# Performance work log

Hardware: AMD Instinct MI355X
Metric: run time of the kernel (lower is better)

The kernel has to match this reference:

```python
import jax, jax.numpy as jnp
import numpy as np

SLOT_DIM = 128
HIDDEN = 64


def setup_inputs() -> dict:
    key = jax.random.key(0)
    k1, k2, k3, k4, k5 = jax.random.split(key, 5)
    b, k, d, h = 64, 128, SLOT_DIM, HIDDEN
    slots = jax.random.normal(k1, (b, k, d), dtype=jnp.float32)
    # edge_mlp params: Linear(2d -> h), Linear(h -> 1)
    s1 = 1.0 / np.sqrt(2 * d)
    W1 = jax.random.uniform(k2, (h, 2 * d), minval=-s1, maxval=s1, dtype=jnp.float32)
    b1 = jax.random.uniform(k3, (h,), minval=-s1, maxval=s1, dtype=jnp.float32)
    s2 = 1.0 / np.sqrt(h)
    W2 = jax.random.uniform(k4, (h,), minval=-s2, maxval=s2, dtype=jnp.float32)
    b2 = jax.random.uniform(k5, (), minval=-s2, maxval=s2, dtype=jnp.float32)
    return {"slots": slots, "W1": W1, "b1": b1, "W2": W2, "b2": b2}


def reference(slots, W1, b1, W2, b2):
    # slots: (b,k,d). Original concatenates [left,right] along features then
    # applies Linear(2d->h). Equivalent (same math): split W1 into halves and
    # broadcast-add, avoiding the (b,k,k,2d) concat tensor.
    b, k, d = slots.shape
    left_h = jnp.einsum('bkd,hd->bkh', slots, W1[:, :d])   # (b,k,h)
    right_h = jnp.einsum('bkd,hd->bkh', slots, W1[:, d:])  # (b,k,h)
    hidden = jax.nn.relu(left_h[:, :, None, :] + right_h[:, None, :, :] + b1)  # (b,k,k,h)
    logits = jnp.einsum('bijh,h->bij', hidden, W2) + b2    # (b,k,k)
    adj = jax.nn.sigmoid(logits)
    eye = jnp.eye(k, dtype=adj.dtype)[None]
    return adj * (1.0 - eye)
```

## Files before the change

### kernel.cpp

```cpp
#include <hip/hip_runtime.h>

#define BB 64
#define KK 128
#define DD 128

typedef __attribute__((ext_vector_type(8))) short bf16x8;
typedef __attribute__((ext_vector_type(4))) float f32x4;
typedef _Float16 half2v __attribute__((ext_vector_type(2)));
typedef __fp16 fp16x2 __attribute__((ext_vector_type(2)));

__device__ __forceinline__ unsigned cvt_pk_bf16(float x, float y) {
    unsigned r;
    asm("v_cvt_pk_bf16_f32 %0, %1, %2" : "=v"(r) : "v"(x), "v"(y));
    return r;
}

__device__ __forceinline__ unsigned cvt_pkrtz_u(float x, float y) {
    const fp16x2 pk = __builtin_amdgcn_cvt_pkrtz(x, y);
    return __builtin_bit_cast(unsigned, pk);
}

__device__ __forceinline__ unsigned pk_add_relu(unsigned a, unsigned b) {
    unsigned s, r;
    asm("v_pk_add_f16 %0, %1, %2" : "=v"(s) : "v"(a), "v"(b));
    asm("v_pk_max_f16 %0, %1, 0" : "=v"(r) : "v"(s));
    return r;
}

__device__ __forceinline__ float dot2acc(unsigned a, unsigned b, float c) {
#if __has_builtin(__builtin_amdgcn_fdot2)
    return __builtin_amdgcn_fdot2(__builtin_bit_cast(half2v, a),
                                  __builtin_bit_cast(half2v, b), c, false);
#else
    float r;
    asm("v_dot2_f32_f16 %0, %1, %2, %3" : "=v"(r) : "v"(a), "v"(b), "v"(c));
    return r;
#endif
}

__global__ __launch_bounds__(512, 2) void fused_kernel(
    const float* __restrict__ slots, const float* __restrict__ W1,
    const float* __restrict__ b1, const float* __restrict__ W2,
    const float* __restrict__ b2p, float* __restrict__ out)
{
    __shared__ unsigned smem_w[16384];
    char* smem = (char*)smem_w;

    const int t   = threadIdx.x;
    const int blk = blockIdx.x;
    const int b   = blk >> 2;
    const int it  = (blk >> 1) & 1;
    const int jt  = blk & 1;

    const int lane = t & 63;
    const int w    = t >> 6;
    const int lr   = lane & 15;
    const int lk   = lane >> 4;
    const int side = w >> 2;
    const int hq   = w & 3;

    const float badd = (side == 0) ? b1[hq * 16 + lr] : 0.0f;
    float w2lo = 0.f, w2hi = 0.f;
    if (t < 32) {
        const int hl = (t & 15) + 32 * (t >> 4);
        w2lo = W2[hl]; w2hi = W2[hl + 16];
    }

    {
        const float* srcI = slots + ((size_t)(b * KK) + it * 64) * DD;
        const float* srcJ = slots + ((size_t)(b * KK) + jt * 64) * DD;
#pragma unroll
        for (int x0 = 0; x0 < 2048; x0 += 512) {
            const int x = x0 + t;
            const int row = x >> 4, cb = x & 15;
            const float* src = (row < 64 ? srcI + row * DD
                                         : srcJ + (row - 64) * DD) + cb * 8;
            const float4 f0 = *reinterpret_cast<const float4*>(src);
            const float4 f1 = *reinterpret_cast<const float4*>(src + 4);
            uint4 pk;
            pk.x = cvt_pk_bf16(f0.x, f0.y); pk.y = cvt_pk_bf16(f0.z, f0.w);
            pk.z = cvt_pk_bf16(f1.x, f1.y); pk.w = cvt_pk_bf16(f1.z, f1.w);
            *reinterpret_cast<uint4*>(smem + row * 256 + ((cb ^ (row & 7)) << 4)) = pk;
        }
#pragma unroll
        for (int x0 = 0; x0 < 2048; x0 += 512) {
            const int x = x0 + t;
            const int row = x >> 5, cb = x & 31;
            const float* src = W1 + row * 256 + cb * 8;
            const float4 f0 = *reinterpret_cast<const float4*>(src);
            const float4 f1 = *reinterpret_cast<const float4*>(src + 4);
            uint4 pk;
            pk.x = cvt_pk_bf16(f0.x, f0.y); pk.y = cvt_pk_bf16(f0.z, f0.w);
            pk.z = cvt_pk_bf16(f1.x, f1.y); pk.w = cvt_pk_bf16(f1.z, f1.w);
            *reinterpret_cast<uint4*>(smem + 32768 + row * 512 + ((cb ^ (row & 7)) << 4)) = pk;
        }
    }
    __syncthreads();

    bf16x8 bfr[4];
#pragma unroll
    for (int kf = 0; kf < 4; ++kf) {
        const int rowB = hq * 16 + lr;
        const int cb   = side * 16 + kf * 4 + lk;
        bfr[kf] = *reinterpret_cast<const bf16x8*>(
            smem + 32768 + rowB * 512 + ((cb ^ (rowB & 7)) << 4));
    }
    f32x4 acc[4];
#pragma unroll
    for (int m = 0; m < 4; ++m) acc[m] = f32x4{0.f, 0.f, 0.f, 0.f};
#pragma unroll
    for (int m = 0; m < 4; ++m) {
#pragma unroll
        for (int kf = 0; kf < 4; ++kf) {
            const int row = side * 64 + 16 * m + lr;
            const int cb  = kf * 4 + lk;
            const bf16x8 af = *reinterpret_cast<const bf16x8*>(
                smem + row * 256 + ((cb ^ (row & 7)) << 4));
            acc[m] = __builtin_amdgcn_mfma_f32_16x16x32_bf16(af, bfr[kf], acc[m], 0, 0, 0);
        }
    }
    __syncthreads();

    {
        __fp16* dst = (__fp16*)smem + (side ? 4608 : 0);
        const int g  = hq >> 1;
        const int hl = hq & 1;
#pragma unroll
        for (int m = 0; m < 4; ++m)
#pragma unroll
            for (int r = 0; r < 4; ++r) {
                const int row = 16 * m + 4 * lk + r;
                dst[(row * 36 + g * 16 + lr) * 2 + hl] = (__fp16)(acc[m][r] + badd);
            }
        if (t < 32) ((unsigned*)smem)[4608 + t] = cvt_pkrtz_u(w2lo, w2hi);
    }
    __syncthreads();

    const int tx = t & 15;
    const int ty = t >> 4;
    const unsigned* LsP = (const unsigned*)smem;
    const unsigned* RsP = LsP + 2304;
    const unsigned* W2p = LsP + 4608;

    uint4 w2r[8];
#pragma unroll
    for (int s = 0; s < 8; ++s)
        w2r[s] = *reinterpret_cast<const uint4*>(W2p + s * 4);

    float pacc[2][4] = {};
    uint4 l4a[2], r4a[4], l4b[2], r4b[4];

#define LD_STEP(L4, R4, s)                                                        \
    {                                                                             \
        _Pragma("unroll") for (int ii = 0; ii < 2; ++ii)                          \
            L4[ii] = *reinterpret_cast<const uint4*>(LsP + (ty + 32 * ii) * 36 + (s) * 4); \
        _Pragma("unroll") for (int jj = 0; jj < 4; ++jj)                          \
            R4[jj] = *reinterpret_cast<const uint4*>(RsP + (tx + 16 * jj) * 36 + (s) * 4); \
    }

#define COMPUTE_STEP(L4, R4, s)                                                   \
    {                                                                             \
        _Pragma("unroll") for (int ii = 0; ii < 2; ++ii)                          \
        _Pragma("unroll") for (int jj = 0; jj < 4; ++jj) {                        \
            float a = pacc[ii][jj];                                               \
            a = dot2acc(pk_add_relu(L4[ii].x, R4[jj].x), w2r[s].x, a);            \
            a = dot2acc(pk_add_relu(L4[ii].y, R4[jj].y), w2r[s].y, a);            \
            a = dot2acc(pk_add_relu(L4[ii].z, R4[jj].z), w2r[s].z, a);            \
            a = dot2acc(pk_add_relu(L4[ii].w, R4[jj].w), w2r[s].w, a);            \
            pacc[ii][jj] = a;                                                     \
        }                                                                         \
    }

    LD_STEP(l4a, r4a, 0)
#pragma unroll
    for (int sp = 0; sp < 4; ++sp) {
        LD_STEP(l4b, r4b, 2 * sp + 1)
        COMPUTE_STEP(l4a, r4a, 2 * sp)
        if (sp < 3) LD_STEP(l4a, r4a, 2 * sp + 2)
        COMPUTE_STEP(l4b, r4b, 2 * sp + 1)
    }
#undef LD_STEP
#undef COMPUTE_STEP

    const float b2 = *b2p;
#pragma unroll
    for (int ii = 0; ii < 2; ++ii) {
        const int gi = it * 64 + ty + 32 * ii;
        float* orow = out + ((size_t)(b * KK) + gi) * KK + jt * 64;
#pragma unroll
        for (int jj = 0; jj < 4; ++jj) {
            const int jl = tx + 16 * jj;
            const int gj = jt * 64 + jl;
            const float xv = pacc[ii][jj] + b2;
            const float sg = 1.0f / (1.0f + __expf(-xv));
            orow[jl] = (gi == gj) ? 0.0f : sg;
        }
    }
}

extern "C" void kernel_launch(void* const* d_in, const int* in_sizes, int n_in,
                              void* d_out, int out_size, void* d_ws, size_t ws_size,
                              hipStream_t stream) {
    const float* slots = (const float*)d_in[0];
    const float* W1    = (const float*)d_in[1];
    const float* b1    = (const float*)d_in[2];
    const float* W2    = (const float*)d_in[3];
    const float* b2    = (const float*)d_in[4];
    float* out = (float*)d_out;
    (void)d_ws; (void)ws_size; (void)in_sizes; (void)n_in; (void)out_size;

    fused_kernel<<<BB * 4, 512, 0, stream>>>(slots, W1, b1, W2, b2, out);
}
```

Measured before the change: 12.56 us.

## Split into 512 smaller blocks with W1 fragments loaded straight to registers

The grid doubles to 512 blocks of 256 threads, each owning a 64x32 output tile instead of 64x64. W1 B-fragments are now loaded from global memory directly into registers, which removes the W1 shared-memory staging and one barrier and shrinks LDS use. Each wave computes two h-column fragments so the MFMA phase covers all 64 hidden units with 4 waves, and the right side only projects its 32 rows. The cost is more redundant projection of the I-side rows and more repeated W1 global reads across blocks.

```diff
diff --git a/kernel.cpp b/kernel.cpp
--- a/kernel.cpp
+++ b/kernel.cpp
@@ -38,39 +38,56 @@
 #endif
 }
 
-__global__ __launch_bounds__(512, 2) void fused_kernel(
+__global__ __launch_bounds__(256, 2) void fused_kernel(
     const float* __restrict__ slots, const float* __restrict__ W1,
     const float* __restrict__ b1, const float* __restrict__ W2,
     const float* __restrict__ b2p, float* __restrict__ out)
 {
-    __shared__ unsigned smem_w[16384];
+    __shared__ unsigned smem_w[9632];
     char* smem = (char*)smem_w;
 
     const int t   = threadIdx.x;
     const int blk = blockIdx.x;
-    const int b   = blk >> 2;
-    const int it  = (blk >> 1) & 1;
-    const int jt  = blk & 1;
+    const int b   = blk >> 3;
+    const int it  = (blk >> 2) & 1;
+    const int jt  = blk & 3;
 
     const int lane = t & 63;
     const int w    = t >> 6;
     const int lr   = lane & 15;
     const int lk   = lane >> 4;
-    const int side = w >> 2;
-    const int hq   = w & 3;
-
-    const float badd = (side == 0) ? b1[hq * 16 + lr] : 0.0f;
+    const int side = w >> 1;
+    const int grp  = w & 1;
+
+    const float b2 = *b2p;
+    const float b1lo = (side == 0) ? b1[grp * 32 + lr]      : 0.0f;
+    const float b1hi = (side == 0) ? b1[grp * 32 + 16 + lr] : 0.0f;
     float w2lo = 0.f, w2hi = 0.f;
     if (t < 32) {
         const int hl = (t & 15) + 32 * (t >> 4);
         w2lo = W2[hl]; w2hi = W2[hl + 16];
     }
 
+    bf16x8 bfr[2][4];
+#pragma unroll
+    for (int n = 0; n < 2; ++n)
+#pragma unroll
+        for (int kf = 0; kf < 4; ++kf) {
+            const int rowB = grp * 32 + n * 16 + lr;
+            const float* p = W1 + rowB * 256 + side * 128 + kf * 32 + lk * 8;
+            const float4 f0 = *reinterpret_cast<const float4*>(p);
+            const float4 f1 = *reinterpret_cast<const float4*>(p + 4);
+            uint4 pk;
+            pk.x = cvt_pk_bf16(f0.x, f0.y); pk.y = cvt_pk_bf16(f0.z, f0.w);
+            pk.z = cvt_pk_bf16(f1.x, f1.y); pk.w = cvt_pk_bf16(f1.z, f1.w);
+            bfr[n][kf] = __builtin_bit_cast(bf16x8, pk);
+        }
+
     {
         const float* srcI = slots + ((size_t)(b * KK) + it * 64) * DD;
-        const float* srcJ = slots + ((size_t)(b * KK) + jt * 64) * DD;
-#pragma unroll
-        for (int x0 = 0; x0 < 2048; x0 += 512) {
+        const float* srcJ = slots + ((size_t)(b * KK) + jt * 32) * DD;
+#pragma unroll
+        for (int x0 = 0; x0 < 1536; x0 += 256) {
             const int x = x0 + t;
             const int row = x >> 4, cb = x & 15;
             const float* src = (row < 64 ? srcI + row * DD
@@ -82,86 +99,73 @@
             pk.z = cvt_pk_bf16(f1.x, f1.y); pk.w = cvt_pk_bf16(f1.z, f1.w);
             *reinterpret_cast<uint4*>(smem + row * 256 + ((cb ^ (row & 7)) << 4)) = pk;
         }
-#pragma unroll
-        for (int x0 = 0; x0 < 2048; x0 += 512) {
-            const int x = x0 + t;
-            const int row = x >> 5, cb = x & 31;
-            const float* src = W1 + row * 256 + cb * 8;
-            const float4 f0 = *reinterpret_cast<const float4*>(src);
-            const float4 f1 = *reinterpret_cast<const float4*>(src + 4);
-            uint4 pk;
-            pk.x = cvt_pk_bf16(f0.x, f0.y); pk.y = cvt_pk_bf16(f0.z, f0.w);
-            pk.z = cvt_pk_bf16(f1.x, f1.y); pk.w = cvt_pk_bf16(f1.z, f1.w);
-            *reinterpret_cast<uint4*>(smem + 32768 + row * 512 + ((cb ^ (row & 7)) << 4)) = pk;
-        }
     }
     __syncthreads();
 
-    bf16x8 bfr[4];
-#pragma unroll
-    for (int kf = 0; kf < 4; ++kf) {
-        const int rowB = hq * 16 + lr;
-        const int cb   = side * 16 + kf * 4 + lk;
-        bfr[kf] = *reinterpret_cast<const bf16x8*>(
-            smem + 32768 + rowB * 512 + ((cb ^ (rowB & 7)) << 4));
-    }
-    f32x4 acc[4];
-#pragma unroll
-    for (int m = 0; m < 4; ++m) acc[m] = f32x4{0.f, 0.f, 0.f, 0.f};
+    f32x4 acc[4][2];
+#pragma unroll
+    for (int m = 0; m < 4; ++m)
+#pragma unroll
+        for (int n = 0; n < 2; ++n) acc[m][n] = f32x4{0.f, 0.f, 0.f, 0.f};
+
 #pragma unroll
     for (int m = 0; m < 4; ++m) {
+        if (side == 1 && m >= 2) continue;
 #pragma unroll
         for (int kf = 0; kf < 4; ++kf) {
             const int row = side * 64 + 16 * m + lr;
             const int cb  = kf * 4 + lk;
             const bf16x8 af = *reinterpret_cast<const bf16x8*>(
                 smem + row * 256 + ((cb ^ (row & 7)) << 4));
-            acc[m] = __builtin_amdgcn_mfma_f32_16x16x32_bf16(af, bfr[kf], acc[m], 0, 0, 0);
-        }
-    }
-    __syncthreads();
+#pragma unroll
+            for (int n = 0; n < 2; ++n)
+                acc[m][n] = __builtin_amdgcn_mfma_f32_16x16x32_bf16(
+                    af, bfr[n][kf], acc[m][n], 0, 0, 0);
+        }
+    }
 
     {
-        __fp16* dst = (__fp16*)smem + (side ? 4608 : 0);
-        const int g  = hq >> 1;
-        const int hl = hq & 1;
-#pragma unroll
-        for (int m = 0; m < 4; ++m)
+        unsigned* dst = smem_w + (side ? 8448 : 6144);
+#pragma unroll
+        for (int m = 0; m < 4; ++m) {
+            if (side == 1 && m >= 2) continue;
 #pragma unroll
             for (int r = 0; r < 4; ++r) {
                 const int row = 16 * m + 4 * lk + r;
-                dst[(row * 36 + g * 16 + lr) * 2 + hl] = (__fp16)(acc[m][r] + badd);
+                dst[row * 36 + grp * 16 + lr] =
+                    cvt_pkrtz_u(acc[m][0][r] + b1lo, acc[m][1][r] + b1hi);
             }
-        if (t < 32) ((unsigned*)smem)[4608 + t] = cvt_pkrtz_u(w2lo, w2hi);
+        }
+        if (t < 32) smem_w[9600 + t] = cvt_pkrtz_u(w2lo, w2hi);
     }
     __syncthreads();
 
     const int tx = t & 15;
     const int ty = t >> 4;
-    const unsigned* LsP = (const unsigned*)smem;
-    const unsigned* RsP = LsP + 2304;
-    const unsigned* W2p = LsP + 4608;
+    const unsigned* LsP = smem_w + 6144;
+    const unsigned* RsP = smem_w + 8448;
+    const unsigned* W2p = smem_w + 9600;
 
     uint4 w2r[8];
 #pragma unroll
     for (int s = 0; s < 8; ++s)
         w2r[s] = *reinterpret_cast<const uint4*>(W2p + s * 4);
 
-    float pacc[2][4] = {};
-    uint4 l4a[2], r4a[4], l4b[2], r4b[4];
+    float pacc[4][2] = {};
+    uint4 l4a[4], r4a[2], l4b[4], r4b[2];
 
 #define LD_STEP(L4, R4, s)                                                        \
     {                                                                             \
-        _Pragma("unroll") for (int ii = 0; ii < 2; ++ii)                          \
-            L4[ii] = *reinterpret_cast<const uint4*>(LsP + (ty + 32 * ii) * 36 + (s) * 4); \
-        _Pragma("unroll") for (int jj = 0; jj < 4; ++jj)                          \
+        _Pragma("unroll") for (int ii = 0; ii < 4; ++ii)                          \
+            L4[ii] = *reinterpret_cast<const uint4*>(LsP + (ty + 16 * ii) * 36 + (s) * 4); \
+        _Pragma("unroll") for (int jj = 0; jj < 2; ++jj)                          \
             R4[jj] = *reinterpret_cast<const uint4*>(RsP + (tx + 16 * jj) * 36 + (s) * 4); \
     }
 
 #define COMPUTE_STEP(L4, R4, s)                                                   \
     {                                                                             \
-        _Pragma("unroll") for (int ii = 0; ii < 2; ++ii)                          \
-        _Pragma("unroll") for (int jj = 0; jj < 4; ++jj) {                        \
+        _Pragma("unroll") for (int ii = 0; ii < 4; ++ii)                          \
+        _Pragma("unroll") for (int jj = 0; jj < 2; ++jj) {                        \
             float a = pacc[ii][jj];                                               \
             a = dot2acc(pk_add_relu(L4[ii].x, R4[jj].x), w2r[s].x, a);            \
             a = dot2acc(pk_add_relu(L4[ii].y, R4[jj].y), w2r[s].y, a);            \
@@ -182,15 +186,14 @@
 #undef LD_STEP
 #undef COMPUTE_STEP
 
-    const float b2 = *b2p;
-#pragma unroll
-    for (int ii = 0; ii < 2; ++ii) {
-        const int gi = it * 64 + ty + 32 * ii;
-        float* orow = out + ((size_t)(b * KK) + gi) * KK + jt * 64;
-#pragma unroll
-        for (int jj = 0; jj < 4; ++jj) {
+#pragma unroll
+    for (int ii = 0; ii < 4; ++ii) {
+        const int gi = it * 64 + ty + 16 * ii;
+        float* orow = out + ((size_t)(b * KK) + gi) * KK + jt * 32;
+#pragma unroll
+        for (int jj = 0; jj < 2; ++jj) {
             const int jl = tx + 16 * jj;
-            const int gj = jt * 64 + jl;
+            const int gj = jt * 32 + jl;
             const float xv = pacc[ii][jj] + b2;
             const float sg = 1.0f / (1.0f + __expf(-xv));
             orow[jl] = (gi == gj) ? 0.0f : sg;
@@ -209,5 +212,5 @@
     float* out = (float*)d_out;
     (void)d_ws; (void)ws_size; (void)in_sizes; (void)n_in; (void)out_size;
 
-    fused_kernel<<<BB * 4, 512, 0, stream>>>(slots, W1, b1, W2, b2, out);
-}
+    fused_kernel<<<BB * 8, 256, 0, stream>>>(slots, W1, b1, W2, b2, out);
+}
```

After: 14.88 us. +18.4%, slower.

## Load W1 fragments directly into registers and retile MFMA to drop a barrier

Applied to the files above, without the earlier changes.

Each wave now loads its W1 B-fragments straight from global memory into registers, so W1 is no longer staged through shared memory. The MFMA work is retiled so each wave computes a 32x32 output block (2x2 fragments) instead of a 64x16 one. The half-precision L/R results go to a separate shared region, which removes the barrier between the MFMA reads and the writes, and a packed conversion replaces the scalar fp16 stores. This shrinks LDS use and removes one synchronization, at the cost of redundant uncoalesced global W1 reads across blocks and more registers held.

```diff
diff --git a/kernel.cpp b/kernel.cpp
--- a/kernel.cpp
+++ b/kernel.cpp
@@ -43,7 +43,7 @@
     const float* __restrict__ b1, const float* __restrict__ W2,
     const float* __restrict__ b2p, float* __restrict__ out)
 {
-    __shared__ unsigned smem_w[16384];
+    __shared__ unsigned smem_w[12832];
     char* smem = (char*)smem_w;
 
     const int t   = threadIdx.x;
@@ -57,14 +57,32 @@
     const int lr   = lane & 15;
     const int lk   = lane >> 4;
     const int side = w >> 2;
-    const int hq   = w & 3;
-
-    const float badd = (side == 0) ? b1[hq * 16 + lr] : 0.0f;
-    float w2lo = 0.f, w2hi = 0.f;
+    const int grp  = (w >> 1) & 1;
+    const int mh   = w & 1;
+
+    const float b2v  = *b2p;
+    const float b1lo = (side == 0) ? b1[grp * 32 + lr]      : 0.0f;
+    const float b1hi = (side == 0) ? b1[grp * 32 + 16 + lr] : 0.0f;
+
     if (t < 32) {
         const int hl = (t & 15) + 32 * (t >> 4);
-        w2lo = W2[hl]; w2hi = W2[hl + 16];
-    }
+        smem_w[12800 + t] = cvt_pkrtz_u(W2[hl], W2[hl + 16]);
+    }
+
+    bf16x8 bfr[2][4];
+#pragma unroll
+    for (int n = 0; n < 2; ++n)
+#pragma unroll
+        for (int kf = 0; kf < 4; ++kf) {
+            const int rowB = grp * 32 + n * 16 + lr;
+            const float* p = W1 + rowB * 256 + side * 128 + kf * 32 + lk * 8;
+            const float4 f0 = *reinterpret_cast<const float4*>(p);
+            const float4 f1 = *reinterpret_cast<const float4*>(p + 4);
+            uint4 pk;
+            pk.x = cvt_pk_bf16(f0.x, f0.y); pk.y = cvt_pk_bf16(f0.z, f0.w);
+            pk.z = cvt_pk_bf16(f1.x, f1.y); pk.w = cvt_pk_bf16(f1.z, f1.w);
+            bfr[n][kf] = __builtin_bit_cast(bf16x8, pk);
+        }
 
     {
         const float* srcI = slots + ((size_t)(b * KK) + it * 64) * DD;
@@ -82,65 +100,45 @@
             pk.z = cvt_pk_bf16(f1.x, f1.y); pk.w = cvt_pk_bf16(f1.z, f1.w);
             *reinterpret_cast<uint4*>(smem + row * 256 + ((cb ^ (row & 7)) << 4)) = pk;
         }
-#pragma unroll
-        for (int x0 = 0; x0 < 2048; x0 += 512) {
-            const int x = x0 + t;
-            const int row = x >> 5, cb = x & 31;
-            const float* src = W1 + row * 256 + cb * 8;
-            const float4 f0 = *reinterpret_cast<const float4*>(src);
-            const float4 f1 = *reinterpret_cast<const float4*>(src + 4);
-            uint4 pk;
-            pk.x = cvt_pk_bf16(f0.x, f0.y); pk.y = cvt_pk_bf16(f0.z, f0.w);
-            pk.z = cvt_pk_bf16(f1.x, f1.y); pk.w = cvt_pk_bf16(f1.z, f1.w);
-            *reinterpret_cast<uint4*>(smem + 32768 + row * 512 + ((cb ^ (row & 7)) << 4)) = pk;
-        }
     }
     __syncthreads();
 
-    bf16x8 bfr[4];
-#pragma unroll
-    for (int kf = 0; kf < 4; ++kf) {
-        const int rowB = hq * 16 + lr;
-        const int cb   = side * 16 + kf * 4 + lk;
-        bfr[kf] = *reinterpret_cast<const bf16x8*>(
-            smem + 32768 + rowB * 512 + ((cb ^ (rowB & 7)) << 4));
-    }
-    f32x4 acc[4];
-#pragma unroll
-    for (int m = 0; m < 4; ++m) acc[m] = f32x4{0.f, 0.f, 0.f, 0.f};
-#pragma unroll
-    for (int m = 0; m < 4; ++m) {
+    f32x4 acc[2][2];
+#pragma unroll
+    for (int m = 0; m < 2; ++m)
+#pragma unroll
+        for (int n = 0; n < 2; ++n) acc[m][n] = f32x4{0.f, 0.f, 0.f, 0.f};
+
+#pragma unroll
+    for (int m = 0; m < 2; ++m)
 #pragma unroll
         for (int kf = 0; kf < 4; ++kf) {
-            const int row = side * 64 + 16 * m + lr;
+            const int row = side * 64 + mh * 32 + m * 16 + lr;
             const int cb  = kf * 4 + lk;
             const bf16x8 af = *reinterpret_cast<const bf16x8*>(
                 smem + row * 256 + ((cb ^ (row & 7)) << 4));
-            acc[m] = __builtin_amdgcn_mfma_f32_16x16x32_bf16(af, bfr[kf], acc[m], 0, 0, 0);
-        }
-    }
-    __syncthreads();
+            acc[m][0] = __builtin_amdgcn_mfma_f32_16x16x32_bf16(af, bfr[0][kf], acc[m][0], 0, 0, 0);
+            acc[m][1] = __builtin_amdgcn_mfma_f32_16x16x32_bf16(af, bfr[1][kf], acc[m][1], 0, 0, 0);
+        }
 
     {
-        __fp16* dst = (__fp16*)smem + (side ? 4608 : 0);
-        const int g  = hq >> 1;
-        const int hl = hq & 1;
-#pragma unroll
-        for (int m = 0; m < 4; ++m)
+        unsigned* dst = smem_w + (side ? 10496 : 8192);
+#pragma unroll
+        for (int m = 0; m < 2; ++m)
 #pragma unroll
             for (int r = 0; r < 4; ++r) {
-                const int row = 16 * m + 4 * lk + r;
-                dst[(row * 36 + g * 16 + lr) * 2 + hl] = (__fp16)(acc[m][r] + badd);
+                const int row = mh * 32 + 16 * m + 4 * lk + r;
+                dst[row * 36 + grp * 16 + lr] =
+                    cvt_pkrtz_u(acc[m][0][r] + b1lo, acc[m][1][r] + b1hi);
             }
-        if (t < 32) ((unsigned*)smem)[4608 + t] = cvt_pkrtz_u(w2lo, w2hi);
     }
     __syncthreads();
 
     const int tx = t & 15;
     const int ty = t >> 4;
-    const unsigned* LsP = (const unsigned*)smem;
-    const unsigned* RsP = LsP + 2304;
-    const unsigned* W2p = LsP + 4608;
+    const unsigned* LsP = smem_w + 8192;
+    const unsigned* RsP = smem_w + 10496;
+    const unsigned* W2p = smem_w + 12800;
 
     uint4 w2r[8];
 #pragma unroll
@@ -182,7 +180,6 @@
 #undef LD_STEP
 #undef COMPUTE_STEP
 
-    const float b2 = *b2p;
 #pragma unroll
     for (int ii = 0; ii < 2; ++ii) {
         const int gi = it * 64 + ty + 32 * ii;
@@ -191,7 +188,7 @@
         for (int jj = 0; jj < 4; ++jj) {
             const int jl = tx + 16 * jj;
             const int gj = jt * 64 + jl;
-            const float xv = pacc[ii][jj] + b2;
+            const float xv = pacc[ii][jj] + b2v;
             const float sg = 1.0f / (1.0f + __expf(-xv));
             orow[jl] = (gi == gj) ? 0.0f : sg;
         }
```

Result: slower. 15.33 us (+22.0%).
